# Kernel optimization log

Measured on AMD Instinct MI355X. Metric: run time of the kernel, lower is better.

Reference implementation:

```python
import jax, jax.numpy as jnp
import numpy as np

V = 32000   # src and trg vocab
E = 512     # embed_dim
H = 1024    # hidden_dim
S = 512     # source length
T = 512     # target length


def _lstm_scan(x_seq, h0, c0, Wih, Whh, bih, bhh):
    """Single-layer LSTM over x_seq [L, E] with PyTorch gate order (i,f,g,o)."""
    def step(carry, x):
        h, c = carry
        gates = x @ Wih.T + bih + h @ Whh.T + bhh  # [4H]
        i, f, g, o = jnp.split(gates, 4)
        i = jax.nn.sigmoid(i)
        f = jax.nn.sigmoid(f)
        g = jnp.tanh(g)
        o = jax.nn.sigmoid(o)
        c = f * c + i * g
        h = o * jnp.tanh(c)
        return (h, c), h
    (h, c), hs = jax.lax.scan(step, (h0, c0), x_seq)
    return hs, (h, c)


def setup_inputs() -> dict:
    key = jax.random.key(0)
    ks = jax.random.split(key, 16)
    s = 0.05
    return {
        "source": jax.random.randint(ks[0], (S,), 0, V),
        "target": jax.random.randint(ks[1], (T,), 0, V),
        # encoder params (embed init uniform(-0.25, 0.25) per source)
        "enc_embed": jax.random.uniform(ks[2], (V, E), jnp.float32, -0.25, 0.25),
        "enc_Wih": jax.random.normal(ks[3], (4 * H, E), jnp.float32) * s,
        "enc_Whh": jax.random.normal(ks[4], (4 * H, H), jnp.float32) * s,
        "enc_bih": jnp.zeros((4 * H,), jnp.float32),
        "enc_bhh": jnp.zeros((4 * H,), jnp.float32),
        # decoder params
        "dec_embed": jax.random.normal(ks[5], (V, E), jnp.float32) * s,
        "dec_Wih": jax.random.normal(ks[6], (4 * H, E), jnp.float32) * s,
        "dec_Whh": jax.random.normal(ks[7], (4 * H, H), jnp.float32) * s,
        "dec_bih": jnp.zeros((4 * H,), jnp.float32),
        "dec_bhh": jnp.zeros((4 * H,), jnp.float32),
        "Wout": jax.random.normal(ks[8], (V, H), jnp.float32) * s,
        "bout": jnp.zeros((V,), jnp.float32),
    }


def reference(source, target, enc_embed, enc_Wih, enc_Whh, enc_bih, enc_bhh,
              dec_embed, dec_Wih, dec_Whh, dec_bih, dec_bhh, Wout, bout):
    # ---- encoder: embed source, run LSTM from zero state, take last h ----
    src_emb = enc_embed[source]                       # [S, E]
    h0 = jnp.zeros((H,), src_emb.dtype)
    c0 = jnp.zeros((H,), src_emb.dtype)
    _, (enc_h, _) = _lstm_scan(src_emb, h0, c0, enc_Wih, enc_Whh, enc_bih, enc_bhh)
    # hidden = (enc_h, tanh(enc_h)) as in original forward
    dh0, dc0 = enc_h, jnp.tanh(enc_h)
    # ---- decoder: teacher-forced over target tokens ----
    trg_emb = dec_embed[target]                       # [T, E]
    hs, _ = _lstm_scan(trg_emb, dh0, dc0, dec_Wih, dec_Whh, dec_bih, dec_bhh)  # [T, H]
    logits = hs @ Wout.T + bout                       # [T, V]
    logp = jax.nn.log_softmax(logits, axis=-1)
    # per-step CrossEntropyLoss(output, target[i]) -> list of T scalar losses
    losses = -jnp.take_along_axis(logp, target[:, None], axis=1)[:, 0]  # [T]
    return losses
```

## Files before the change

kernel.cpp:

```cpp
#include <hip/hip_runtime.h>
#include <cstdint>
#include <cstddef>

#define V_ 32000
#define E_ 512
#define H_ 1024
#define S_ 512
#define T_ 512
#define G4 4096

typedef unsigned long long u64;

__device__ __forceinline__ float fexp2(float x) { return __builtin_amdgcn_exp2f(x); }
__device__ __forceinline__ float sigm(float x) {
  return __builtin_amdgcn_rcpf(1.0f + fexp2(x * -1.442695041f));
}
__device__ __forceinline__ float ftanh(float x) {
  return 2.0f * __builtin_amdgcn_rcpf(1.0f + fexp2(x * -2.885390082f)) - 1.0f;
}

__global__ __launch_bounds__(256) void xi_gemm(
    const float* __restrict__ emb, const int* __restrict__ tok,
    const float* __restrict__ Wih, const float* __restrict__ b1,
    const float* __restrict__ b2, float* __restrict__ Xi) {
  __shared__ float As[32][68];
  __shared__ float Bs[32][68];
  __shared__ int ids[64];
  const int tid = threadIdx.x;
  const int tx = tid & 15, ty = tid >> 4;
  const int t0 = blockIdx.y * 64, r0 = blockIdx.x * 64;
  if (tid < 64) ids[tid] = tok[t0 + tid];
  __syncthreads();
  const int lrow = tid >> 2;
  const int lk   = (tid & 3) * 8;
  const long arow = (long)ids[lrow] * E_;
  const long brow = (long)(r0 + lrow) * E_;
  float acc[4][4] = {};
  for (int k0 = 0; k0 < E_; k0 += 32) {
    float4 a0 = *(const float4*)(emb + arow + k0 + lk);
    float4 a1 = *(const float4*)(emb + arow + k0 + lk + 4);
    float4 w0 = *(const float4*)(Wih + brow + k0 + lk);
    float4 w1 = *(const float4*)(Wih + brow + k0 + lk + 4);
    __syncthreads();
    As[lk + 0][lrow] = a0.x; As[lk + 1][lrow] = a0.y; As[lk + 2][lrow] = a0.z; As[lk + 3][lrow] = a0.w;
    As[lk + 4][lrow] = a1.x; As[lk + 5][lrow] = a1.y; As[lk + 6][lrow] = a1.z; As[lk + 7][lrow] = a1.w;
    Bs[lk + 0][lrow] = w0.x; Bs[lk + 1][lrow] = w0.y; Bs[lk + 2][lrow] = w0.z; Bs[lk + 3][lrow] = w0.w;
    Bs[lk + 4][lrow] = w1.x; Bs[lk + 5][lrow] = w1.y; Bs[lk + 6][lrow] = w1.z; Bs[lk + 7][lrow] = w1.w;
    __syncthreads();
#pragma unroll
    for (int kk = 0; kk < 32; ++kk) {
      float4 av = *(const float4*)&As[kk][ty * 4];
      float4 bv = *(const float4*)&Bs[kk][tx * 4];
      float a_[4] = {av.x, av.y, av.z, av.w};
      float b_[4] = {bv.x, bv.y, bv.z, bv.w};
#pragma unroll
      for (int i = 0; i < 4; ++i)
#pragma unroll
        for (int j = 0; j < 4; ++j) acc[i][j] += a_[i] * b_[j];
    }
  }
#pragma unroll
  for (int i = 0; i < 4; ++i) {
    const int t = t0 + ty * 4 + i;
#pragma unroll
    for (int j = 0; j < 4; ++j) {
      const int r = r0 + tx * 4 + j;
      Xi[(size_t)t * G4 + r] = acc[i][j] + b1[r] + b2[r];
    }
  }
}

__global__ __launch_bounds__(1024, 4) void lstm_seq(
    const float* __restrict__ Xi_enc, const float* __restrict__ Xi_dec,
    const float* __restrict__ Whh_enc, const float* __restrict__ Whh_dec,
    u64* __restrict__ hpair,
    float* __restrict__ hs) {
  __shared__ float h_lds[2][16 * 68 + 4];
  __shared__ float gh[16];
  const int tid = threadIdx.x;
  const int wg = blockIdx.x;
  const int wv = tid >> 6;
  const int ln = tid & 63;
  const int g  = ln >> 4;
  const int c  = ln & 15;
  const int unit = wg * 16 + wv;
  const int grow = g * H_ + unit;
  const int c64 = c * 64;

  float4 w[16];
  {
    const float* wp = Whh_enc + (size_t)grow * H_ + c64;
#pragma unroll
    for (int q = 0; q < 16; ++q) w[q] = *(const float4*)(wp + q * 4);
  }
  const float* Xi = Xi_enc;
  float cstate = 0.f, h_own = 0.f;
  int dead = 0;

  for (int s = 0; s < 1024; ++s) {
    if (s == 512) {
      const float* wp = Whh_dec + (size_t)grow * H_ + c64;
#pragma unroll
      for (int q = 0; q < 16; ++q) w[q] = *(const float4*)(wp + q * 4);
      Xi = Xi_dec;
      cstate = ftanh(h_own);
    }
    float xi = 0.f;
    if (c == 0) xi = Xi[(size_t)(s & 511) * G4 + grow];

    const u64* pb = hpair + (size_t)(s & 1) * H_;
    const unsigned want = (unsigned)s;
    u64 p;
    {
      int tries = 0;
      for (;;) {
        p = __hip_atomic_load(pb + tid, __ATOMIC_RELAXED, __HIP_MEMORY_SCOPE_AGENT);
        bool ok = ((unsigned)(p >> 32) == want);
        if (__ballot(ok) == ~0ull || dead) break;
        if (++tries > (1 << 20)) { dead = 1; break; }
        __builtin_amdgcn_s_sleep(1);
      }
    }
    float* buf = h_lds[s & 1];
    buf[wv * 68 + ln] = __uint_as_float((unsigned)p);
    __syncthreads();

    float acc = 0.f;
    const float* hb = &buf[c * 68];
#pragma unroll
    for (int q = 0; q < 16; ++q) {
      float4 h4 = *(const float4*)(hb + q * 4);
      acc += w[q].x * h4.x + w[q].y * h4.y + w[q].z * h4.z + w[q].w * h4.w;
    }
    acc += __shfl_xor(acc, 8, 64);
    acc += __shfl_xor(acc, 4, 64);
    acc += __shfl_xor(acc, 2, 64);
    acc += __shfl_xor(acc, 1, 64);
    float val = acc + xi;

    float act = (g == 2) ? ftanh(val) : sigm(val);
    float i_ = __shfl(act, 0, 64);
    float f_ = __shfl(act, 16, 64);
    float g_ = __shfl(act, 32, 64);
    float o_ = __shfl(act, 48, 64);
    cstate = f_ * cstate + i_ * g_;
    float h = o_ * ftanh(cstate);
    h_own = h;
    if (ln == 0) gh[wv] = h;
    __syncthreads();

    if (wv == 0 && ln < 16) {
      float hv = gh[ln];
      const int k = wg * 16 + ln;
      u64 pair = ((u64)(unsigned)(s + 1) << 32) | (u64)__float_as_uint(hv);
      __hip_atomic_store(hpair + (size_t)((s + 1) & 1) * H_ + k, pair,
                         __ATOMIC_RELAXED, __HIP_MEMORY_SCOPE_AGENT);
      if (s >= 512) hs[(size_t)(s - 512) * H_ + k] = hv;
    }
  }
}

#define PHYS(j) ((j) + (((j) >> 5) << 2))

__global__ __launch_bounds__(256) void logits_lse(
    const float* __restrict__ hs, const float* __restrict__ Wout,
    const float* __restrict__ bout, const int* __restrict__ tgt,
    float* __restrict__ pmax, float* __restrict__ psum,
    float* __restrict__ tgtlog) {
  __shared__ float As[32][140];
  __shared__ float Bs[32][140];
  __shared__ float red[128][17];
  __shared__ float Mlds[128];
  __shared__ int tg[128];
  const int tid = threadIdx.x;
  const int tx = tid & 15, ty = tid >> 4;
  const int t0 = blockIdx.y * 128, v0 = blockIdx.x * 128;
  if (tid < 128) tg[tid] = tgt[t0 + tid];
  const int lrow = tid >> 1;
  const int lk   = (tid & 1) * 16;
  const float* ap = hs + (size_t)(t0 + lrow) * H_ + lk;
  const float* bp = Wout + (size_t)(v0 + lrow) * H_ + lk;
  const int pl = PHYS(lrow);
  const int aoff = PHYS(ty * 8);
  const int boff = PHYS(tx * 8);
  float acc[8][8] = {};
  for (int k0 = 0; k0 < H_; k0 += 32) {
    float4 a[4], b[4];
#pragma unroll
    for (int q = 0; q < 4; ++q) {
      a[q] = *(const float4*)(ap + k0 + q * 4);
      b[q] = *(const float4*)(bp + k0 + q * 4);
    }
    __syncthreads();
#pragma unroll
    for (int q = 0; q < 4; ++q) {
      As[lk + q * 4 + 0][pl] = a[q].x; As[lk + q * 4 + 1][pl] = a[q].y;
      As[lk + q * 4 + 2][pl] = a[q].z; As[lk + q * 4 + 3][pl] = a[q].w;
      Bs[lk + q * 4 + 0][pl] = b[q].x; Bs[lk + q * 4 + 1][pl] = b[q].y;
      Bs[lk + q * 4 + 2][pl] = b[q].z; Bs[lk + q * 4 + 3][pl] = b[q].w;
    }
    __syncthreads();
#pragma unroll
    for (int kk = 0; kk < 32; ++kk) {
      float av[8], bv[8];
      *(float4*)&av[0] = *(const float4*)&As[kk][aoff];
      *(float4*)&av[4] = *(const float4*)&As[kk][aoff + 4];
      *(float4*)&bv[0] = *(const float4*)&Bs[kk][boff];
      *(float4*)&bv[4] = *(const float4*)&Bs[kk][boff + 4];
#pragma unroll
      for (int i = 0; i < 8; ++i)
#pragma unroll
        for (int j = 0; j < 8; ++j) acc[i][j] += av[i] * bv[j];
    }
  }
  float bv8[8];
#pragma unroll
  for (int j = 0; j < 8; ++j) bv8[j] = bout[v0 + tx * 8 + j];
#pragma unroll
  for (int i = 0; i < 8; ++i) {
    float m = -3.0e38f;
#pragma unroll
    for (int j = 0; j < 8; ++j) {
      acc[i][j] += bv8[j];
      m = fmaxf(m, acc[i][j]);
    }
    red[ty * 8 + i][tx] = m;
  }
  __syncthreads();
  if (tid < 128) {
    float M = -3.0e38f;
#pragma unroll
    for (int x = 0; x < 16; ++x) M = fmaxf(M, red[tid][x]);
    Mlds[tid] = M;
  }
  __syncthreads();
#pragma unroll
  for (int i = 0; i < 8; ++i) {
    float M = Mlds[ty * 8 + i];
    float ssum = 0.f;
#pragma unroll
    for (int j = 0; j < 8; ++j) ssum += expf(acc[i][j] - M);
    red[ty * 8 + i][tx] = ssum;
  }
  __syncthreads();
  if (tid < 128) {
    float S = 0.f;
#pragma unroll
    for (int x = 0; x < 16; ++x) S += red[tid][x];
    pmax[(size_t)(t0 + tid) * 250 + blockIdx.x] = Mlds[tid];
    psum[(size_t)(t0 + tid) * 250 + blockIdx.x] = S;
  }
#pragma unroll
  for (int i = 0; i < 8; ++i) {
    const int t = t0 + ty * 8 + i;
    const int loc = tg[ty * 8 + i] - v0 - tx * 8;
    if (loc >= 0 && loc < 8) {
#pragma unroll
      for (int j = 0; j < 8; ++j)
        if (j == loc) tgtlog[t] = acc[i][j];
    }
  }
}

__global__ __launch_bounds__(256) void reduce_loss(
    const float* __restrict__ pmax, const float* __restrict__ psum,
    const float* __restrict__ tgtlog, float* __restrict__ out) {
  __shared__ float sm[256];
  __shared__ float ss[256];
  const int t = blockIdx.x, tid = threadIdx.x;
  float m = -3.0e38f;
  if (tid < 250) m = pmax[(size_t)t * 250 + tid];
  sm[tid] = m;
  __syncthreads();
  for (int s = 128; s > 0; s >>= 1) {
    if (tid < s) sm[tid] = fmaxf(sm[tid], sm[tid + s]);
    __syncthreads();
  }
  const float M = sm[0];
  float sv = 0.f;
  if (tid < 250) sv = psum[(size_t)t * 250 + tid] * expf(m - M);
  ss[tid] = sv;
  __syncthreads();
  for (int s = 128; s > 0; s >>= 1) {
    if (tid < s) ss[tid] += ss[tid + s];
    __syncthreads();
  }
  if (tid == 0) out[t] = M + logf(ss[0]) - tgtlog[t];
}

extern "C" void kernel_launch(void* const* d_in, const int* in_sizes, int n_in,
                              void* d_out, int out_size, void* d_ws, size_t ws_size,
                              hipStream_t stream) {
  const int*   source    = (const int*)  d_in[0];
  const int*   target    = (const int*)  d_in[1];
  const float* enc_embed = (const float*)d_in[2];
  const float* enc_Wih   = (const float*)d_in[3];
  const float* enc_Whh   = (const float*)d_in[4];
  const float* enc_bih   = (const float*)d_in[5];
  const float* enc_bhh   = (const float*)d_in[6];
  const float* dec_embed = (const float*)d_in[7];
  const float* dec_Wih   = (const float*)d_in[8];
  const float* dec_Whh   = (const float*)d_in[9];
  const float* dec_bih   = (const float*)d_in[10];
  const float* dec_bhh   = (const float*)d_in[11];
  const float* Wout      = (const float*)d_in[12];
  const float* bout      = (const float*)d_in[13];
  float* out = (float*)d_out;

  char* ws = (char*)d_ws;
  float* Xi_enc = (float*)(ws);
  float* Xi_dec = (float*)(ws + 8388608);
  float* hs     = (float*)(ws + 16777216);
  u64*   hpair  = (u64*)  (ws + 18874368);
  float* pmax   = (float*)(ws + 18890752);
  float* psum   = (float*)(ws + 19402752);
  float* tgtlog = (float*)(ws + 19914752);

  hipMemsetAsync((void*)hpair, 0, 2 * H_ * sizeof(u64), stream);
  xi_gemm<<<dim3(64, 8), 256, 0, stream>>>(enc_embed, source, enc_Wih, enc_bih, enc_bhh, Xi_enc);
  xi_gemm<<<dim3(64, 8), 256, 0, stream>>>(dec_embed, target, dec_Wih, dec_bih, dec_bhh, Xi_dec);
  lstm_seq<<<64, 1024, 0, stream>>>(Xi_enc, Xi_dec, enc_Whh, dec_Whh, hpair, hs);
  logits_lse<<<dim3(250, 4), 256, 0, stream>>>(hs, Wout, bout, target, pmax, psum, tgtlog);
  reduce_loss<<<512, 256, 0, stream>>>(pmax, psum, tgtlog, out);
}
```

Baseline: 2.647 ms.

## Remove block barriers from LSTM recurrence using per-wave global polling and tagged LDS handoff

```diff
diff --git a/kernel.cpp b/kernel.cpp
--- a/kernel.cpp
+++ b/kernel.cpp
@@ -75,70 +75,84 @@
     const float* __restrict__ Whh_enc, const float* __restrict__ Whh_dec,
     u64* __restrict__ hpair,
     float* __restrict__ hs) {
-  __shared__ float h_lds[2][16 * 68 + 4];
-  __shared__ float gh[16];
+  __shared__ u64 gh[16];
   const int tid = threadIdx.x;
   const int wg = blockIdx.x;
   const int wv = tid >> 6;
   const int ln = tid & 63;
-  const int g  = ln >> 4;
-  const int c  = ln & 15;
+  const int grp = ln >> 4;
   const int unit = wg * 16 + wv;
-  const int grow = g * H_ + unit;
-  const int c64 = c * 64;
-
-  float4 w[16];
-  {
-    const float* wp = Whh_enc + (size_t)grow * H_ + c64;
-#pragma unroll
-    for (int q = 0; q < 16; ++q) w[q] = *(const float4*)(wp + q * 4);
-  }
+
+  float w[64];
+#pragma unroll
+  for (int g = 0; g < 4; ++g)
+#pragma unroll
+    for (int q = 0; q < 16; ++q)
+      w[g * 16 + q] = Whh_enc[(size_t)(g * H_ + unit) * H_ + q * 64 + ln];
+
+  if (tid < 16) gh[tid] = 0;
+  __syncthreads();
+
   const float* Xi = Xi_enc;
   float cstate = 0.f, h_own = 0.f;
   int dead = 0;
 
   for (int s = 0; s < 1024; ++s) {
     if (s == 512) {
-      const float* wp = Whh_dec + (size_t)grow * H_ + c64;
-#pragma unroll
-      for (int q = 0; q < 16; ++q) w[q] = *(const float4*)(wp + q * 4);
+#pragma unroll
+      for (int g = 0; g < 4; ++g)
+#pragma unroll
+        for (int q = 0; q < 16; ++q)
+          w[g * 16 + q] = Whh_dec[(size_t)(g * H_ + unit) * H_ + q * 64 + ln];
       Xi = Xi_dec;
       cstate = ftanh(h_own);
     }
-    float xi = 0.f;
-    if (c == 0) xi = Xi[(size_t)(s & 511) * G4 + grow];
+    float xi = Xi[(size_t)(s & 511) * G4 + grp * H_ + unit];
 
     const u64* pb = hpair + (size_t)(s & 1) * H_;
     const unsigned want = (unsigned)s;
-    u64 p;
+    u64 pr[16];
+    unsigned done = 0;
     {
       int tries = 0;
-      for (;;) {
-        p = __hip_atomic_load(pb + tid, __ATOMIC_RELAXED, __HIP_MEMORY_SCOPE_AGENT);
-        bool ok = ((unsigned)(p >> 32) == want);
-        if (__ballot(ok) == ~0ull || dead) break;
-        if (++tries > (1 << 20)) { dead = 1; break; }
+      while (done != 0xFFFFu && !dead) {
+#pragma unroll
+        for (int q = 0; q < 16; ++q)
+          if (!((done >> q) & 1))
+            pr[q] = __hip_atomic_load(pb + q * 64 + ln, __ATOMIC_RELAXED,
+                                      __HIP_MEMORY_SCOPE_AGENT);
+#pragma unroll
+        for (int q = 0; q < 16; ++q)
+          if (!((done >> q) & 1)) {
+            bool ok = ((unsigned)(pr[q] >> 32) == want);
+            if (__ballot(ok) == ~0ull) done |= (1u << q);
+          }
+        if (done == 0xFFFFu) break;
+        if (++tries > (1 << 18)) { dead = 1; break; }
         __builtin_amdgcn_s_sleep(1);
       }
     }
-    float* buf = h_lds[s & 1];
-    buf[wv * 68 + ln] = __uint_as_float((unsigned)p);
-    __syncthreads();
-
-    float acc = 0.f;
-    const float* hb = &buf[c * 68];
+
+    float acc0 = 0.f, acc1 = 0.f, acc2 = 0.f, acc3 = 0.f;
 #pragma unroll
     for (int q = 0; q < 16; ++q) {
-      float4 h4 = *(const float4*)(hb + q * 4);
-      acc += w[q].x * h4.x + w[q].y * h4.y + w[q].z * h4.z + w[q].w * h4.w;
-    }
-    acc += __shfl_xor(acc, 8, 64);
-    acc += __shfl_xor(acc, 4, 64);
-    acc += __shfl_xor(acc, 2, 64);
-    acc += __shfl_xor(acc, 1, 64);
-    float val = acc + xi;
-
-    float act = (g == 2) ? ftanh(val) : sigm(val);
+      float hq = __uint_as_float((unsigned)pr[q]);
+      acc0 += w[0 * 16 + q] * hq;
+      acc1 += w[1 * 16 + q] * hq;
+      acc2 += w[2 * 16 + q] * hq;
+      acc3 += w[3 * 16 + q] * hq;
+    }
+    acc0 += __shfl_xor(acc0, 16, 64); acc0 += __shfl_xor(acc0, 32, 64);
+    acc1 += __shfl_xor(acc1, 16, 64); acc1 += __shfl_xor(acc1, 32, 64);
+    acc2 += __shfl_xor(acc2, 16, 64); acc2 += __shfl_xor(acc2, 32, 64);
+    acc3 += __shfl_xor(acc3, 16, 64); acc3 += __shfl_xor(acc3, 32, 64);
+    float val = (grp == 0) ? acc0 : (grp == 1) ? acc1 : (grp == 2) ? acc2 : acc3;
+    val += __shfl_xor(val, 8, 64);
+    val += __shfl_xor(val, 4, 64);
+    val += __shfl_xor(val, 2, 64);
+    val += __shfl_xor(val, 1, 64);
+    val += xi;
+    float act = (grp == 2) ? ftanh(val) : sigm(val);
     float i_ = __shfl(act, 0, 64);
     float f_ = __shfl(act, 16, 64);
     float g_ = __shfl(act, 32, 64);
@@ -146,16 +160,26 @@
     cstate = f_ * cstate + i_ * g_;
     float h = o_ * ftanh(cstate);
     h_own = h;
-    if (ln == 0) gh[wv] = h;
-    __syncthreads();
-
-    if (wv == 0 && ln < 16) {
-      float hv = gh[ln];
-      const int k = wg * 16 + ln;
-      u64 pair = ((u64)(unsigned)(s + 1) << 32) | (u64)__float_as_uint(hv);
-      __hip_atomic_store(hpair + (size_t)((s + 1) & 1) * H_ + k, pair,
-                         __ATOMIC_RELAXED, __HIP_MEMORY_SCOPE_AGENT);
-      if (s >= 512) hs[(size_t)(s - 512) * H_ + k] = hv;
+
+    if (ln == 0)
+      ((volatile u64*)gh)[wv] = ((u64)(unsigned)(s + 1) << 32) | (u64)__float_as_uint(h);
+
+    if (wv == 0) {
+      const unsigned wnext = (unsigned)(s + 1);
+      u64 gp;
+      int t2 = 0;
+      for (;;) {
+        gp = ((volatile u64*)gh)[ln & 15];
+        bool ok = ((unsigned)(gp >> 32) == wnext);
+        if (__ballot(ok) == ~0ull || dead) break;
+        if (++t2 > (1 << 18)) { dead = 1; break; }
+      }
+      if (ln < 16) {
+        __hip_atomic_store(hpair + (size_t)((s + 1) & 1) * H_ + wg * 16 + ln, gp,
+                           __ATOMIC_RELAXED, __HIP_MEMORY_SCOPE_AGENT);
+        if (s >= 512)
+          hs[(size_t)(s - 512) * H_ + wg * 16 + ln] = __uint_as_float((unsigned)gp);
+      }
     }
   }
 }
```

Result: slower. 8.608 ms (+225.2%).
